# Optimization experiments

Hardware: AMD Instinct MI355X
Metric: run time of the kernel (lower is better)

## Reference

```python
import jax, jax.numpy as jnp
import numpy as np

EPS = 1e-7  # K.epsilon()
ROUTINGS = 3


def squash(v, axis=-1):
    s2 = jnp.sum(jnp.square(v), axis=axis, keepdims=True)
    scale = s2 / (1.0 + s2) / jnp.sqrt(s2 + EPS)
    return scale * v


def setup_inputs() -> dict:
    key = jax.random.key(0)
    k1, k2 = jax.random.split(key)
    B, Ni, Di, No, Do = 64, 2048, 16, 32, 16
    inputs = jax.random.normal(k1, (B, Ni, Di), dtype=jnp.float32)
    # glorot-uniform-ish scale for W
    limit = np.sqrt(6.0 / (Di + Do)).astype(np.float32)
    W = jax.random.uniform(k2, (1, Ni, No, Do, Di), dtype=jnp.float32,
                           minval=-limit, maxval=limit)
    return {"inputs": inputs, "W": W}


def reference(inputs, W):
    # inputs: [B, Ni, Di]; W: [1, Ni, No, Do, Di]
    # inputs_hat[b,n,o,d] = sum_i W[n,o,d,i] * inputs[b,n,i]  -> [B, Ni, No, Do]
    inputs_hat = jnp.einsum('bni,nodi->bnod', inputs, W[0])
    B, Ni, No, _ = inputs_hat.shape
    b = jnp.zeros((B, Ni, No), dtype=inputs_hat.dtype)
    outputs = None
    for i in range(ROUTINGS):
        c = jax.nn.softmax(b, axis=2)              # [B, Ni, No]
        s = jnp.einsum('bnod,bno->bod', inputs_hat, c)  # weighted sum over Ni
        outputs = squash(s)                        # [B, No, Do]
        if i < ROUTINGS - 1:
            # NOTE: faithful to source — update uses sum over Do of c-weighted
            # inputs_hat (does NOT use `outputs`).
            b = b + jnp.sum(inputs_hat * c[..., None], axis=-1)
    return outputs
```

## Files before the change

kernel.cpp:

```cpp
#include <hip/hip_runtime.h>
#include <cmath>


#define NI 2048

typedef short bf16x8 __attribute__((ext_vector_type(8)));
typedef float f32x4 __attribute__((ext_vector_type(4)));

static __device__ __forceinline__ unsigned short f2bf(float f) {
  unsigned u = __float_as_uint(f);
  u += 0x7FFFu + ((u >> 16) & 1u);
  return (unsigned short)(u >> 16);
}
static __device__ __forceinline__ float bf2f(unsigned short h) {
  return __uint_as_float(((unsigned)h) << 16);
}
static __device__ __forceinline__ void split4(float4 v, uint2& hi, uint2& lo) {
  unsigned short h0 = f2bf(v.x), h1 = f2bf(v.y), h2 = f2bf(v.z), h3 = f2bf(v.w);
  unsigned short l0 = f2bf(v.x - bf2f(h0)), l1 = f2bf(v.y - bf2f(h1));
  unsigned short l2 = f2bf(v.z - bf2f(h2)), l3 = f2bf(v.w - bf2f(h3));
  hi.x = (unsigned)h0 | ((unsigned)h1 << 16); hi.y = (unsigned)h2 | ((unsigned)h3 << 16);
  lo.x = (unsigned)l0 | ((unsigned)l1 << 16); lo.y = (unsigned)l2 | ((unsigned)l3 << 16);
}

__global__ __launch_bounds__(256) void caps_c2_kernel(
    const float* __restrict__ x, const float* __restrict__ W,
    float* __restrict__ c2g)
{
  const int n = blockIdx.x;
  const int t = threadIdx.x;
  const int wv = t >> 6, l = t & 63;
  __shared__ __align__(16) float WdS[32 * 20];
  __shared__ float xs[64 * 17];
  __shared__ float c2s[64 * 33];

  {
    const int d = l >> 2, i4 = l & 3;
    #pragma unroll
    for (int m = 0; m < 8; ++m) {
      const int o = m * 4 + wv;
      float4 v = *(const float4*)(W + (size_t)n * 8192 + o * 256 + d * 16 + i4 * 4);
      float s0 = v.x, s1 = v.y, s2 = v.z, s3 = v.w;
      #pragma unroll
      for (int mk = 4; mk <= 32; mk <<= 1) {
        s0 += __shfl_xor(s0, mk); s1 += __shfl_xor(s1, mk);
        s2 += __shfl_xor(s2, mk); s3 += __shfl_xor(s3, mk);
      }
      if (l < 4) *(float4*)&WdS[o * 20 + l * 4] = make_float4(s0, s1, s2, s3);
    }
  }
  {
    const int i = t & 15;
    #pragma unroll
    for (int m = 0; m < 4; ++m) {
      int b = m * 16 + (t >> 4);
      xs[b * 17 + i] = x[(size_t)b * (NI * 16) + n * 16 + i];
    }
  }
  __syncthreads();

  {
    const int b = t >> 2, oq = t & 3;
    float h[8];
    #pragma unroll
    for (int jj = 0; jj < 8; ++jj) {
      const int o = oq + 4 * jj;
      float acc = 0.f;
      #pragma unroll
      for (int i = 0; i < 16; ++i) acc += WdS[o * 20 + i] * xs[b * 17 + i];
      h[jj] = acc;
    }
    float b1[8], e[8];
    float mx = -1e30f;
    #pragma unroll
    for (int jj = 0; jj < 8; ++jj) { b1[jj] = h[jj] * 0.03125f; mx = fmaxf(mx, b1[jj]); }
    mx = fmaxf(mx, __shfl_xor(mx, 1)); mx = fmaxf(mx, __shfl_xor(mx, 2));
    float S = 0.f;
    #pragma unroll
    for (int jj = 0; jj < 8; ++jj) { e[jj] = __expf(b1[jj] - mx); S += e[jj]; }
    S += __shfl_xor(S, 1); S += __shfl_xor(S, 2);
    float inv = 1.0f / S;
    float b2[8]; float mx2 = -1e30f;
    #pragma unroll
    for (int jj = 0; jj < 8; ++jj) { b2[jj] = b1[jj] + e[jj] * inv * h[jj]; mx2 = fmaxf(mx2, b2[jj]); }
    mx2 = fmaxf(mx2, __shfl_xor(mx2, 1)); mx2 = fmaxf(mx2, __shfl_xor(mx2, 2));
    float S2 = 0.f;
    #pragma unroll
    for (int jj = 0; jj < 8; ++jj) { e[jj] = __expf(b2[jj] - mx2); S2 += e[jj]; }
    S2 += __shfl_xor(S2, 1); S2 += __shfl_xor(S2, 2);
    float inv2 = 1.0f / S2;
    #pragma unroll
    for (int jj = 0; jj < 8; ++jj) c2s[b * 33 + oq + 4 * jj] = e[jj] * inv2;
  }
  __syncthreads();
  #pragma unroll
  for (int m = 0; m < 8; ++m) {
    int flat = m * 256 + t;
    c2g[(size_t)n * 2048 + flat] = c2s[(flat & 63) * 33 + (flat >> 6)];
  }
}

#define WAOFF 0
#define XBOFF 6144
#define C2OFF 7680
__global__ __launch_bounds__(512, 4) void caps_main_kernel(
    const float* __restrict__ x, const float* __restrict__ W,
    const float* __restrict__ c2, float* __restrict__ partial)
{
  const int bx = blockIdx.x;
  const int ng = bx >> 1, hh = bx & 1;
  const int t = threadIdx.x;
  const int wv = t >> 6, l = t & 63;
  const int q = l >> 4, dq = l & 15, qh = q & 1, s_a = q >> 1;
  const int bt = wv & 3, oct = wv >> 2;

  __shared__ __align__(16) float lds[8704];
  float* WA  = lds + WAOFF;
  float* XB  = lds + XBOFF;
  float* C2L = lds + C2OFF;

  float sacc[8][4];
  #pragma unroll
  for (int oo = 0; oo < 8; ++oo)
    { sacc[oo][0] = 0.f; sacc[oo][1] = 0.f; sacc[oo][2] = 0.f; sacc[oo][3] = 0.f; }

  const int n0 = ng * 8;
  const int wo = t >> 6;
  const int wd = (t >> 2) & 15, wi4 = t & 3;
  const int xb = t >> 3, xi = (t & 7) * 2;

  float4 wreg0 = *(const float4*)(W + (size_t)n0 * 8192 + hh * 4096 + 4 * t);
  float4 wreg1 = *(const float4*)(W + (size_t)n0 * 8192 + hh * 4096 + 4 * (t + 512));
  float2 xreg  = *(const float2*)(x + (size_t)xb * (NI * 16) + n0 * 16 + xi);
  float2 creg  = *(const float2*)(c2 + (size_t)n0 * 2048 + hh * 1024 + 2 * t);

  #pragma unroll 1
  for (int nn = 0; nn < 8; ++nn) {
    {
      uint2 hi, lo;
      split4(wreg0, hi, lo);
      int row = (wo * 32 + wd) * 12;
      *(uint2*)((char*)&WA[row] + wi4 * 8) = hi;
      *(uint2*)((char*)&WA[row + 16 * 12] + wi4 * 8) = lo;
      split4(wreg1, hi, lo);
      row = ((wo + 8) * 32 + wd) * 12;
      *(uint2*)((char*)&WA[row] + wi4 * 8) = hi;
      *(uint2*)((char*)&WA[row + 16 * 12] + wi4 * 8) = lo;
      unsigned short h0 = f2bf(xreg.x), h1 = f2bf(xreg.y);
      unsigned short g0 = f2bf(xreg.x - bf2f(h0)), g1 = f2bf(xreg.y - bf2f(h1));
      ((unsigned*)&XB[xb * 12])[xi >> 1]            = (unsigned)h0 | ((unsigned)h1 << 16);
      ((unsigned*)&XB[(64 + xb) * 12])[xi >> 1]     = (unsigned)g0 | ((unsigned)g1 << 16);
      *(float2*)&C2L[2 * t] = creg;
    }
    __syncthreads();

    if (nn < 7) {
      const size_t nb = (size_t)(n0 + nn + 1);
      wreg0 = *(const float4*)(W + nb * 8192 + hh * 4096 + 4 * t);
      wreg1 = *(const float4*)(W + nb * 8192 + hh * 4096 + 4 * (t + 512));
      xreg  = *(const float2*)(x + (size_t)xb * (NI * 16) + nb * 16 + xi);
      creg  = *(const float2*)(c2 + nb * 2048 + hh * 1024 + 2 * t);
    }

    bf16x8 B0 = *(const bf16x8*)&XB[(bt * 16 + dq) * 12 + qh * 4];
    bf16x8 B1 = *(const bf16x8*)&XB[(64 + bt * 16 + dq) * 12 + qh * 4];
    #pragma unroll
    for (int oo = 0; oo < 8; ++oo) {
      const int o = oct * 8 + oo;
      bf16x8 A = *(const bf16x8*)&WA[(o * 32 + s_a * 16 + dq) * 12 + qh * 4];
      f32x4 D = {0.f, 0.f, 0.f, 0.f};
      D = __builtin_amdgcn_mfma_f32_16x16x32_bf16(A, B0, D, 0, 0, 0);
      D = __builtin_amdgcn_mfma_f32_16x16x32_bf16(A, B1, D, 0, 0, 0);
      float c = C2L[o * 64 + bt * 16 + dq];
      sacc[oo][0] += c * D[0]; sacc[oo][1] += c * D[1];
      sacc[oo][2] += c * D[2]; sacc[oo][3] += c * D[3];
    }
    __syncthreads();
  }

  #pragma unroll
  for (int oo = 0; oo < 8; ++oo) {
    const int o = oct * 8 + oo;
    *(float4*)(partial + (size_t)ng * 32768 + (size_t)(bt * 16 + dq) * 512
               + (hh * 16 + o) * 16 + q * 4)
        = make_float4(sacc[oo][0], sacc[oo][1], sacc[oo][2], sacc[oo][3]);
  }
}

__global__ __launch_bounds__(256) void caps_reduce_kernel(
    const float* __restrict__ partial, float* __restrict__ out)
{
  const int t = threadIdx.x;
  const int w4 = t >> 6, ln = t & 63;
  const int pair = blockIdx.x * 4 + w4;
  const int b = pair >> 5, o = pair & 31;
  const int d = ln & 15, cg = ln >> 4;
  const float* p = partial + (size_t)b * 512 + o * 16 + d;
  float s = 0.f;
  #pragma unroll 8
  for (int gg = cg; gg < 256; gg += 4) s += p[(size_t)gg * 32768];
  s += __shfl_xor(s, 16); s += __shfl_xor(s, 32);
  float s2 = s * s;
  s2 += __shfl_xor(s2, 1); s2 += __shfl_xor(s2, 2);
  s2 += __shfl_xor(s2, 4); s2 += __shfl_xor(s2, 8);
  float scale = s2 / (1.0f + s2) / sqrtf(s2 + 1e-7f);
  if (ln < 16) out[(size_t)b * 512 + o * 16 + d] = scale * s;
}

extern "C" void kernel_launch(void* const* d_in, const int* in_sizes, int n_in,
                              void* d_out, int out_size, void* d_ws, size_t ws_size,
                              hipStream_t stream) {
  const float* x = (const float*)d_in[0];
  const float* W = (const float*)d_in[1];
  if (in_sizes[0] != 64 * 2048 * 16) { const float* tmp = x; x = W; W = tmp; }
  float* out = (float*)d_out;

  float* partial = (float*)d_ws;
  float* c2g     = partial + (size_t)256 * 32768;

  caps_c2_kernel<<<2048, 256, 0, stream>>>(x, W, c2g);
  caps_main_kernel<<<512, 512, 0, stream>>>(x, W, c2g, partial);
  caps_reduce_kernel<<<512, 256, 0, stream>>>(partial, out);
}
```

Before: 137.2 us.

## Fuse routing-coefficient computation into main MFMA kernel, split blocks by batch half

Removes the separate c2 kernel and its global round trip by computing the Do-summed inputs_hat from the MFMA results in-block, then running the two-step softmax in LDS before accumulating. Blocks are now split by batch half instead of output-capsule half, and each block loads the full W slice for its capsule group. The partial layout and the reduce indexing change to match. This adds two extra barriers per iteration and duplicates W loads across the batch halves.

```diff
diff --git a/kernel.cpp b/kernel.cpp
--- a/kernel.cpp
+++ b/kernel.cpp
@@ -15,174 +15,148 @@
 static __device__ __forceinline__ float bf2f(unsigned short h) {
   return __uint_as_float(((unsigned)h) << 16);
 }
-static __device__ __forceinline__ void split4(float4 v, uint2& hi, uint2& lo) {
-  unsigned short h0 = f2bf(v.x), h1 = f2bf(v.y), h2 = f2bf(v.z), h3 = f2bf(v.w);
-  unsigned short l0 = f2bf(v.x - bf2f(h0)), l1 = f2bf(v.y - bf2f(h1));
-  unsigned short l2 = f2bf(v.z - bf2f(h2)), l3 = f2bf(v.w - bf2f(h3));
-  hi.x = (unsigned)h0 | ((unsigned)h1 << 16); hi.y = (unsigned)h2 | ((unsigned)h3 << 16);
-  lo.x = (unsigned)l0 | ((unsigned)l1 << 16); lo.y = (unsigned)l2 | ((unsigned)l3 << 16);
-}
 
-__global__ __launch_bounds__(256) void caps_c2_kernel(
+#define WA_OFF  0
+#define XB0_OFF 8192
+#define XB1_OFF 8704
+#define HS_OFF  9216
+#define C2_OFF  10272
+#define LDS_DW  11328
+
+__global__ __launch_bounds__(512, 4) void caps_fused_kernel(
     const float* __restrict__ x, const float* __restrict__ W,
-    float* __restrict__ c2g)
+    float* __restrict__ partial)
 {
-  const int n = blockIdx.x;
+  const int bid = blockIdx.x;
+  const int ng = ((bid >> 4) << 3) | (bid & 7);
+  const int bh = (bid >> 3) & 1;
   const int t = threadIdx.x;
   const int wv = t >> 6, l = t & 63;
-  __shared__ __align__(16) float WdS[32 * 20];
-  __shared__ float xs[64 * 17];
-  __shared__ float c2s[64 * 33];
+  const int q = l >> 4, dq = l & 15;
+  const int bt = wv & 1, og = wv >> 1;
 
-  {
-    const int d = l >> 2, i4 = l & 3;
-    #pragma unroll
-    for (int m = 0; m < 8; ++m) {
-      const int o = m * 4 + wv;
-      float4 v = *(const float4*)(W + (size_t)n * 8192 + o * 256 + d * 16 + i4 * 4);
-      float s0 = v.x, s1 = v.y, s2 = v.z, s3 = v.w;
-      #pragma unroll
-      for (int mk = 4; mk <= 32; mk <<= 1) {
-        s0 += __shfl_xor(s0, mk); s1 += __shfl_xor(s1, mk);
-        s2 += __shfl_xor(s2, mk); s3 += __shfl_xor(s3, mk);
-      }
-      if (l < 4) *(float4*)&WdS[o * 20 + l * 4] = make_float4(s0, s1, s2, s3);
-    }
-  }
-  {
-    const int i = t & 15;
-    #pragma unroll
-    for (int m = 0; m < 4; ++m) {
-      int b = m * 16 + (t >> 4);
-      xs[b * 17 + i] = x[(size_t)b * (NI * 16) + n * 16 + i];
-    }
-  }
-  __syncthreads();
-
-  {
-    const int b = t >> 2, oq = t & 3;
-    float h[8];
-    #pragma unroll
-    for (int jj = 0; jj < 8; ++jj) {
-      const int o = oq + 4 * jj;
-      float acc = 0.f;
-      #pragma unroll
-      for (int i = 0; i < 16; ++i) acc += WdS[o * 20 + i] * xs[b * 17 + i];
-      h[jj] = acc;
-    }
-    float b1[8], e[8];
-    float mx = -1e30f;
-    #pragma unroll
-    for (int jj = 0; jj < 8; ++jj) { b1[jj] = h[jj] * 0.03125f; mx = fmaxf(mx, b1[jj]); }
-    mx = fmaxf(mx, __shfl_xor(mx, 1)); mx = fmaxf(mx, __shfl_xor(mx, 2));
-    float S = 0.f;
-    #pragma unroll
-    for (int jj = 0; jj < 8; ++jj) { e[jj] = __expf(b1[jj] - mx); S += e[jj]; }
-    S += __shfl_xor(S, 1); S += __shfl_xor(S, 2);
-    float inv = 1.0f / S;
-    float b2[8]; float mx2 = -1e30f;
-    #pragma unroll
-    for (int jj = 0; jj < 8; ++jj) { b2[jj] = b1[jj] + e[jj] * inv * h[jj]; mx2 = fmaxf(mx2, b2[jj]); }
-    mx2 = fmaxf(mx2, __shfl_xor(mx2, 1)); mx2 = fmaxf(mx2, __shfl_xor(mx2, 2));
-    float S2 = 0.f;
-    #pragma unroll
-    for (int jj = 0; jj < 8; ++jj) { e[jj] = __expf(b2[jj] - mx2); S2 += e[jj]; }
-    S2 += __shfl_xor(S2, 1); S2 += __shfl_xor(S2, 2);
-    float inv2 = 1.0f / S2;
-    #pragma unroll
-    for (int jj = 0; jj < 8; ++jj) c2s[b * 33 + oq + 4 * jj] = e[jj] * inv2;
-  }
-  __syncthreads();
-  #pragma unroll
-  for (int m = 0; m < 8; ++m) {
-    int flat = m * 256 + t;
-    c2g[(size_t)n * 2048 + flat] = c2s[(flat & 63) * 33 + (flat >> 6)];
-  }
-}
-
-#define WAOFF 0
-#define XBOFF 6144
-#define C2OFF 7680
-__global__ __launch_bounds__(512, 4) void caps_main_kernel(
-    const float* __restrict__ x, const float* __restrict__ W,
-    const float* __restrict__ c2, float* __restrict__ partial)
-{
-  const int bx = blockIdx.x;
-  const int ng = bx >> 1, hh = bx & 1;
-  const int t = threadIdx.x;
-  const int wv = t >> 6, l = t & 63;
-  const int q = l >> 4, dq = l & 15, qh = q & 1, s_a = q >> 1;
-  const int bt = wv & 3, oct = wv >> 2;
-
-  __shared__ __align__(16) float lds[8704];
-  float* WA  = lds + WAOFF;
-  float* XB  = lds + XBOFF;
-  float* C2L = lds + C2OFF;
+  __shared__ __align__(16) float lds[LDS_DW];
 
   float sacc[8][4];
   #pragma unroll
   for (int oo = 0; oo < 8; ++oo)
-    { sacc[oo][0] = 0.f; sacc[oo][1] = 0.f; sacc[oo][2] = 0.f; sacc[oo][3] = 0.f; }
+    { sacc[oo][0]=0.f; sacc[oo][1]=0.f; sacc[oo][2]=0.f; sacc[oo][3]=0.f; }
 
   const int n0 = ng * 8;
-  const int wo = t >> 6;
   const int wd = (t >> 2) & 15, wi4 = t & 3;
-  const int xb = t >> 3, xi = (t & 7) * 2;
+  const int xb = t >> 3, xip = t & 7;
+  const int xbg = bh * 32 + xb;
 
-  float4 wreg0 = *(const float4*)(W + (size_t)n0 * 8192 + hh * 4096 + 4 * t);
-  float4 wreg1 = *(const float4*)(W + (size_t)n0 * 8192 + hh * 4096 + 4 * (t + 512));
-  float2 xreg  = *(const float2*)(x + (size_t)xb * (NI * 16) + n0 * 16 + xi);
-  float2 creg  = *(const float2*)(c2 + (size_t)n0 * 2048 + hh * 1024 + 2 * t);
+  float4 wreg[4];
+  #pragma unroll
+  for (int j = 0; j < 4; ++j)
+    wreg[j] = *(const float4*)(W + (size_t)n0 * 8192 + 4 * (t + 512 * j));
+  float2 xreg = make_float2(0.f, 0.f);
+  if (t < 256)
+    xreg = *(const float2*)(x + (size_t)xbg * (NI * 16) + n0 * 16 + xip * 2);
 
   #pragma unroll 1
   for (int nn = 0; nn < 8; ++nn) {
     {
-      uint2 hi, lo;
-      split4(wreg0, hi, lo);
-      int row = (wo * 32 + wd) * 12;
-      *(uint2*)((char*)&WA[row] + wi4 * 8) = hi;
-      *(uint2*)((char*)&WA[row + 16 * 12] + wi4 * 8) = lo;
-      split4(wreg1, hi, lo);
-      row = ((wo + 8) * 32 + wd) * 12;
-      *(uint2*)((char*)&WA[row] + wi4 * 8) = hi;
-      *(uint2*)((char*)&WA[row + 16 * 12] + wi4 * 8) = lo;
+      const int Lh = ((wi4 >> 1) << 4) + wd;
+      const int doff = (wi4 & 1) << 1;
+      #pragma unroll
+      for (int j = 0; j < 4; ++j) {
+        const int o = wv + (j << 3);
+        unsigned short h0=f2bf(wreg[j].x), h1=f2bf(wreg[j].y),
+                       h2=f2bf(wreg[j].z), h3=f2bf(wreg[j].w);
+        unsigned short g0=f2bf(wreg[j].x-bf2f(h0)), g1=f2bf(wreg[j].y-bf2f(h1)),
+                       g2=f2bf(wreg[j].z-bf2f(h2)), g3=f2bf(wreg[j].w-bf2f(h3));
+        uint2 hi; hi.x = (unsigned)h0 | ((unsigned)h1<<16); hi.y = (unsigned)h2 | ((unsigned)h3<<16);
+        uint2 lo; lo.x = (unsigned)g0 | ((unsigned)g1<<16); lo.y = (unsigned)g2 | ((unsigned)g3<<16);
+        *(uint2*)&lds[WA_OFF + (o << 8) + (Lh << 2) + doff] = hi;
+        *(uint2*)&lds[WA_OFF + (o << 8) + ((Lh + 32) << 2) + doff] = lo;
+      }
+    }
+    if (t < 256) {
       unsigned short h0 = f2bf(xreg.x), h1 = f2bf(xreg.y);
       unsigned short g0 = f2bf(xreg.x - bf2f(h0)), g1 = f2bf(xreg.y - bf2f(h1));
-      ((unsigned*)&XB[xb * 12])[xi >> 1]            = (unsigned)h0 | ((unsigned)h1 << 16);
-      ((unsigned*)&XB[(64 + xb) * 12])[xi >> 1]     = (unsigned)g0 | ((unsigned)g1 << 16);
-      *(float2*)&C2L[2 * t] = creg;
+      unsigned hw = (unsigned)h0 | ((unsigned)h1 << 16);
+      unsigned lw = (unsigned)g0 | ((unsigned)g1 << 16);
+      const int btx = xb >> 4, dqx = xb & 15;
+      const int a0 = (btx << 8) + ((((xip >> 2) << 4) + dqx) << 2) + (xip & 3);
+      unsigned* B0 = (unsigned*)&lds[XB0_OFF];
+      unsigned* B1 = (unsigned*)&lds[XB1_OFF];
+      B0[a0] = hw; B0[a0 + 128] = hw;
+      B1[a0] = lw; B1[a0 + 128] = lw;
     }
     __syncthreads();
 
     if (nn < 7) {
-      const size_t nb = (size_t)(n0 + nn + 1);
-      wreg0 = *(const float4*)(W + nb * 8192 + hh * 4096 + 4 * t);
-      wreg1 = *(const float4*)(W + nb * 8192 + hh * 4096 + 4 * (t + 512));
-      xreg  = *(const float2*)(x + (size_t)xb * (NI * 16) + nb * 16 + xi);
-      creg  = *(const float2*)(c2 + nb * 2048 + hh * 1024 + 2 * t);
+      #pragma unroll
+      for (int j = 0; j < 4; ++j)
+        wreg[j] = *(const float4*)(W + (size_t)(n0 + nn + 1) * 8192 + 4 * (t + 512 * j));
+      if (t < 256)
+        xreg = *(const float2*)(x + (size_t)xbg * (NI * 16) + (n0 + nn + 1) * 16 + xip * 2);
     }
 
-    bf16x8 B0 = *(const bf16x8*)&XB[(bt * 16 + dq) * 12 + qh * 4];
-    bf16x8 B1 = *(const bf16x8*)&XB[(64 + bt * 16 + dq) * 12 + qh * 4];
+    f32x4 D[8];
+    {
+      bf16x8 B0f = *(const bf16x8*)&lds[XB0_OFF + (bt << 8) + (l << 2)];
+      bf16x8 B1f = *(const bf16x8*)&lds[XB1_OFF + (bt << 8) + (l << 2)];
+      #pragma unroll
+      for (int oo = 0; oo < 8; ++oo) {
+        const int o = (og << 3) + oo;
+        bf16x8 A = *(const bf16x8*)&lds[WA_OFF + (o << 8) + (l << 2)];
+        f32x4 d0 = {0.f, 0.f, 0.f, 0.f};
+        d0 = __builtin_amdgcn_mfma_f32_16x16x32_bf16(A, B0f, d0, 0, 0, 0);
+        d0 = __builtin_amdgcn_mfma_f32_16x16x32_bf16(A, B1f, d0, 0, 0, 0);
+        D[oo] = d0;
+        float hs = d0[0] + d0[1] + d0[2] + d0[3];
+        hs += __shfl_xor(hs, 16);
+        hs += __shfl_xor(hs, 32);
+        if (q == 0) lds[HS_OFF + o * 33 + (bt << 4) + dq] = hs;
+      }
+    }
+    __syncthreads();
+
+    if (t < 256) {
+      const int bl = t >> 3, oq = t & 7;
+      float h[4], b1[4], e[4];
+      #pragma unroll
+      for (int jj = 0; jj < 4; ++jj) h[jj] = lds[HS_OFF + (oq + (jj << 3)) * 33 + bl];
+      float mx = -1e30f;
+      #pragma unroll
+      for (int jj = 0; jj < 4; ++jj) { b1[jj] = h[jj] * 0.03125f; mx = fmaxf(mx, b1[jj]); }
+      mx = fmaxf(mx, __shfl_xor(mx, 1)); mx = fmaxf(mx, __shfl_xor(mx, 2)); mx = fmaxf(mx, __shfl_xor(mx, 4));
+      float S = 0.f;
+      #pragma unroll
+      for (int jj = 0; jj < 4; ++jj) { e[jj] = __expf(b1[jj] - mx); S += e[jj]; }
+      S += __shfl_xor(S, 1); S += __shfl_xor(S, 2); S += __shfl_xor(S, 4);
+      float inv = 1.0f / S;
+      float b2[4]; float mx2 = -1e30f;
+      #pragma unroll
+      for (int jj = 0; jj < 4; ++jj) { b2[jj] = b1[jj] + e[jj] * inv * h[jj]; mx2 = fmaxf(mx2, b2[jj]); }
+      mx2 = fmaxf(mx2, __shfl_xor(mx2, 1)); mx2 = fmaxf(mx2, __shfl_xor(mx2, 2)); mx2 = fmaxf(mx2, __shfl_xor(mx2, 4));
+      float S2 = 0.f;
+      #pragma unroll
+      for (int jj = 0; jj < 4; ++jj) { e[jj] = __expf(b2[jj] - mx2); S2 += e[jj]; }
+      S2 += __shfl_xor(S2, 1); S2 += __shfl_xor(S2, 2); S2 += __shfl_xor(S2, 4);
+      float inv2 = 1.0f / S2;
+      #pragma unroll
+      for (int jj = 0; jj < 4; ++jj) lds[C2_OFF + (oq + (jj << 3)) * 33 + bl] = e[jj] * inv2;
+    }
+    __syncthreads();
+
     #pragma unroll
     for (int oo = 0; oo < 8; ++oo) {
-      const int o = oct * 8 + oo;
-      bf16x8 A = *(const bf16x8*)&WA[(o * 32 + s_a * 16 + dq) * 12 + qh * 4];
-      f32x4 D = {0.f, 0.f, 0.f, 0.f};
-      D = __builtin_amdgcn_mfma_f32_16x16x32_bf16(A, B0, D, 0, 0, 0);
-      D = __builtin_amdgcn_mfma_f32_16x16x32_bf16(A, B1, D, 0, 0, 0);
-      float c = C2L[o * 64 + bt * 16 + dq];
-      sacc[oo][0] += c * D[0]; sacc[oo][1] += c * D[1];
-      sacc[oo][2] += c * D[2]; sacc[oo][3] += c * D[3];
+      const int o = (og << 3) + oo;
+      float c = lds[C2_OFF + o * 33 + (bt << 4) + dq];
+      sacc[oo][0] += c * D[oo][0]; sacc[oo][1] += c * D[oo][1];
+      sacc[oo][2] += c * D[oo][2]; sacc[oo][3] += c * D[oo][3];
     }
-    __syncthreads();
   }
 
+  const size_t slab = (size_t)((ng << 1) | bh) * 16384;
   #pragma unroll
   for (int oo = 0; oo < 8; ++oo) {
-    const int o = oct * 8 + oo;
-    *(float4*)(partial + (size_t)ng * 32768 + (size_t)(bt * 16 + dq) * 512
-               + (hh * 16 + o) * 16 + q * 4)
+    const int o = (og << 3) + oo;
+    *(float4*)(partial + slab + (size_t)((bt << 4) + dq) * 512 + o * 16 + (q << 2))
         = make_float4(sacc[oo][0], sacc[oo][1], sacc[oo][2], sacc[oo][3]);
   }
 }
@@ -195,7 +169,8 @@
   const int pair = blockIdx.x * 4 + w4;
   const int b = pair >> 5, o = pair & 31;
   const int d = ln & 15, cg = ln >> 4;
-  const float* p = partial + (size_t)b * 512 + o * 16 + d;
+  const float* p = partial + (size_t)(b >> 5) * 16384
+                 + (size_t)(b & 31) * 512 + o * 16 + d;
   float s = 0.f;
   #pragma unroll 8
   for (int gg = cg; gg < 256; gg += 4) s += p[(size_t)gg * 32768];
@@ -216,9 +191,7 @@
   float* out = (float*)d_out;
 
   float* partial = (float*)d_ws;
-  float* c2g     = partial + (size_t)256 * 32768;
 
-  caps_c2_kernel<<<2048, 256, 0, stream>>>(x, W, c2g);
-  caps_main_kernel<<<512, 512, 0, stream>>>(x, W, c2g, partial);
+  caps_fused_kernel<<<512, 512, 0, stream>>>(x, W, partial);
   caps_reduce_kernel<<<512, 256, 0, stream>>>(partial, out);
 }
```

After: 137.3 us. About the same (+0.1%).
